# Kernel optimization log

Measured on AMD Instinct MI355X. Metric: run time of the kernel, lower is better.

Reference implementation:

```python
import jax, jax.numpy as jnp
import numpy as np

D_FEAT = 6
T = 64
HID = 128
N = 8192
EPS = 1e-5


def setup_inputs() -> dict:
    key = jax.random.key(0)
    ks = jax.random.split(key, 16)
    s = 0.08
    rn = lambda k, shape: jax.random.normal(k, shape, dtype=jnp.float32) * s
    return {
        "x": jax.random.normal(ks[0], (N, D_FEAT * T), dtype=jnp.float32),
        "w_ih0": rn(ks[1], (3 * HID, D_FEAT)),
        "w_hh0": rn(ks[2], (3 * HID, HID)),
        "b_ih0": rn(ks[3], (3 * HID,)),
        "b_hh0": rn(ks[4], (3 * HID,)),
        "w_ih1": rn(ks[5], (3 * HID, HID)),
        "w_hh1": rn(ks[6], (3 * HID, HID)),
        "b_ih1": rn(ks[7], (3 * HID,)),
        "b_hh1": rn(ks[8], (3 * HID,)),
        "bn1_g": jnp.ones((HID,), jnp.float32),
        "bn1_b": jnp.zeros((HID,), jnp.float32),
        "fc_w": rn(ks[9], (HID, HID)),
        "fc_b": rn(ks[10], (HID,)),
        "bn2_g": jnp.ones((HID,), jnp.float32),
        "bn2_b": jnp.zeros((HID,), jnp.float32),
        "fco_w": rn(ks[11], (1, HID)),
        "fco_b": rn(ks[12], (1,)),
    }


def _gru_layer(xs, w_ih, w_hh, b_ih, b_hh):
    # xs: [T, N, in] -> per-step hidden states [T, N, H] (torch nn.GRU math)
    H = w_hh.shape[1]
    gi_all = jnp.einsum('tni,gi->tng', xs, w_ih) + b_ih  # precompute input gates [T,N,3H]

    def step(h, gi):
        gh = h @ w_hh.T + b_hh
        i_r, i_z, i_n = jnp.split(gi, 3, axis=1)
        h_r, h_z, h_n = jnp.split(gh, 3, axis=1)
        r = jax.nn.sigmoid(i_r + h_r)
        z = jax.nn.sigmoid(i_z + h_z)
        n = jnp.tanh(i_n + r * h_n)
        h_new = (1.0 - z) * n + z * h
        return h_new, h_new

    h0 = jnp.zeros((xs.shape[1], H), dtype=xs.dtype)
    _, hs = jax.lax.scan(step, h0, gi_all)
    return hs


def _bn(x, g, b):
    # BatchNorm1d with track_running_stats=False: always uses batch stats
    mu = jnp.mean(x, axis=0)
    var = jnp.mean((x - mu) ** 2, axis=0)
    return (x - mu) * jax.lax.rsqrt(var + EPS) * g + b


def reference(x, w_ih0, w_hh0, b_ih0, b_hh0, w_ih1, w_hh1, b_ih1, b_hh1,
              bn1_g, bn1_b, fc_w, fc_b, bn2_g, bn2_b, fco_w, fco_b):
    n = x.shape[0]
    # reshape(N, d_feat, T).permute(0,2,1) -> time-major [T, N, d_feat] for scan
    xs = x.reshape(n, D_FEAT, T).transpose(2, 0, 1)
    h1 = _gru_layer(xs, w_ih0, w_hh0, b_ih0, b_hh0)
    h2 = _gru_layer(h1, w_ih1, w_hh1, b_ih1, b_hh1)
    hidden = _bn(h2[-1], bn1_g, bn1_b)  # [N, H]
    # cal_attention: mean_d(h_i * h_j) - mean(h_i)*mean(h_j)
    #   == (hidden @ hidden.T)/H - outer(row_means, row_means)  (exact identity)
    m = jnp.mean(hidden, axis=1)
    att = hidden @ hidden.T / jnp.float32(hidden.shape[1]) - jnp.outer(m, m)  # [N, N]
    out = att @ hidden              # [N, H]
    out = out @ fc_w.T + fc_b
    out = _bn(out, bn2_g, bn2_b)
    out = jax.nn.leaky_relu(out, 0.01)
    return (out @ fco_w.T + fco_b).squeeze(-1)  # [N]
```

## Files before the change

kernel.cpp:

```cpp
#include <hip/hip_runtime.h>

typedef unsigned short u16;
typedef short bf16x8 __attribute__((ext_vector_type(8)));
typedef float f32x4 __attribute__((ext_vector_type(4)));

#define NBATCH 8192

__device__ __forceinline__ f32x4 mfma16(bf16x8 a, bf16x8 b, f32x4 c) {
  return __builtin_amdgcn_mfma_f32_16x16x32_bf16(a, b, c, 0, 0, 0);
}
__device__ __forceinline__ u16 f2bf(float f) {
  unsigned int u = __float_as_uint(f);
  return (u16)((u + 0x7FFFu + ((u >> 16) & 1u)) >> 16);
}
__device__ __forceinline__ float bf2f(u16 h) {
  return __uint_as_float(((unsigned int)h) << 16);
}
__device__ __forceinline__ float sigm(float x) {
  return __builtin_amdgcn_rcpf(1.f + __builtin_amdgcn_exp2f(-1.44269504f * x));
}
__device__ __forceinline__ float tanh_(float x) {
  float t = __builtin_amdgcn_exp2f(2.88539008f * x);
  return 1.f - 2.f * __builtin_amdgcn_rcpf(t + 1.f);
}
__device__ __forceinline__ bf16x8 pack8(const float* p) {
  float4 a = *(const float4*)p, b = *(const float4*)(p + 4);
  bf16x8 r;
  r[0] = (short)f2bf(a.x); r[1] = (short)f2bf(a.y);
  r[2] = (short)f2bf(a.z); r[3] = (short)f2bf(a.w);
  r[4] = (short)f2bf(b.x); r[5] = (short)f2bf(b.y);
  r[6] = (short)f2bf(b.z); r[7] = (short)f2bf(b.w);
  return r;
}


#define A_WHH0 0
#define A_H0B  98304
#define A_XB   114688
#define A_LDS  118784

#define GRU0_STEP(RD, WR, T)                                                    \
  {                                                                             \
    if (xact && (T) < 63) {                                                     \
      u16 xh = f2bf(xv);                                                        \
      u16 xl = f2bf(xv - bf2f(xh));                                             \
      char* xw = sm + A_XB + (WR)*2048 + xm*64 + xd*2;                          \
      *(u16*)xw = xh; *(u16*)(xw + 16) = xl; *(u16*)(xw + 32) = xh;             \
      if ((T) < 62) xv = gx[(T) + 2];                                           \
    }                                                                           \
    f32x4 rz0[2][2], hn0[2], in0[2];                                            \
    _Pragma("unroll") for (int mt = 0; mt < 2; ++mt) {                          \
      rz0[mt][0] = (f32x4){brz0r, brz0r, brz0r, brz0r};                         \
      rz0[mt][1] = (f32x4){brz0z, brz0z, brz0z, brz0z};                         \
      hn0[mt] = (f32x4){bhn0, bhn0, bhn0, bhn0};                                \
      in0[mt] = (f32x4){bin0, bin0, bin0, bin0};                                \
    }                                                                           \
    _Pragma("unroll") for (int ki = 0; ki < 4; ++ki) {                          \
      bf16x8 a0 = *(bf16x8*)(sm + A_H0B + (RD)*8192 + arow0 + ad[ki]);          \
      bf16x8 a1 = *(bf16x8*)(sm + A_H0B + (RD)*8192 + arow1 + ad[ki]);          \
      bf16x8 b0 = *(bf16x8*)(sm + brow0 + ad[ki]);                              \
      bf16x8 b1 = *(bf16x8*)(sm + brow1 + ad[ki]);                              \
      bf16x8 b2 = *(bf16x8*)(sm + brow2 + ad[ki]);                              \
      rz0[0][0] = mfma16(a0, b0, rz0[0][0]);                                    \
      rz0[0][1] = mfma16(a0, b1, rz0[0][1]);                                    \
      hn0[0]    = mfma16(a0, b2, hn0[0]);                                       \
      rz0[1][0] = mfma16(a1, b0, rz0[1][0]);                                    \
      rz0[1][1] = mfma16(a1, b1, rz0[1][1]);                                    \
      hn0[1]    = mfma16(a1, b2, hn0[1]);                                       \
    }                                                                           \
    {                                                                           \
      bf16x8 ax0 = *(bf16x8*)(sm + A_XB + (RD)*2048 + xr0);                     \
      bf16x8 ax1 = *(bf16x8*)(sm + A_XB + (RD)*2048 + xr1);                     \
      rz0[0][0] = mfma16(ax0, wf0a, rz0[0][0]);                                 \
      rz0[0][1] = mfma16(ax0, wf0b, rz0[0][1]);                                 \
      in0[0]    = mfma16(ax0, wf0c, in0[0]);                                    \
      rz0[1][0] = mfma16(ax1, wf0a, rz0[1][0]);                                 \
      rz0[1][1] = mfma16(ax1, wf0b, rz0[1][1]);                                 \
      in0[1]    = mfma16(ax1, wf0c, in0[1]);                                    \
    }                                                                           \
    if ((T) >= 1) {       \
      uint4 gv = *(const uint4*)(sm + A_H0B + (RD)*8192 + tid*16);              \
      *(uint4*)(h0seq + (size_t)((T)-1)*2097152 + gofs) = gv;                   \
    }                                                                           \
    _Pragma("unroll") for (int mt = 0; mt < 2; ++mt)                            \
    _Pragma("unroll") for (int r = 0; r < 4; ++r) {                             \
      int s = mt*4 + r;                                                         \
      float rr = sigm(rz0[mt][0][r]);                                           \
      float zz = sigm(rz0[mt][1][r]);                                           \
      float nn = tanh_(__builtin_fmaf(rr, hn0[mt][r], in0[mt][r]));             \
      float h = h0s[s]; h = __builtin_fmaf(zz, h - nn, nn); h0s[s] = h;         \
      *(u16*)(sm + A_H0B + (WR)*8192 + st[s]) = f2bf(h);                        \
    }                                                                           \
    __syncthreads();                                                            \
  }

__global__ __attribute__((amdgpu_flat_work_group_size(512, 512)))
void k_gru0(const float* __restrict__ x,
            const float* __restrict__ wih0, const float* __restrict__ whh0,
            const float* __restrict__ bih0, const float* __restrict__ bhh0,
            char* __restrict__ h0seq) {
  extern __shared__ char sm[];
  const int tid = threadIdx.x;
  const int wid = tid >> 6;
  const int lane = tid & 63;
  const int lq = lane >> 4;
  const int ul = lane & 15;
  const int u  = wid * 16 + ul;
  const int n0 = blockIdx.x * 32;
  const int sx = (ul & 7) << 4;
  const int gofs = blockIdx.x * 8192 + tid * 16;

  for (int idx = tid; idx < 5120; idx += 512)
    *(float*)(sm + A_H0B + idx * 4) = 0.f;
  for (int idx = tid; idx < 12288; idx += 512) {
    int g = idx >> 5, c4 = (idx & 31) * 4;
    float4 v = *(const float4*)(whh0 + g * 128 + c4);
    unsigned int p0 = (unsigned int)f2bf(v.x) | ((unsigned int)f2bf(v.y) << 16);
    unsigned int p1 = (unsigned int)f2bf(v.z) | ((unsigned int)f2bf(v.w) << 16);
    unsigned int* dst = (unsigned int*)(sm + A_WHH0 + g * 256 + ((c4 * 2) ^ ((g & 7) << 4)));
    dst[0] = p0; dst[1] = p1;
  }

  bf16x8 wf0a, wf0b, wf0c;
  {
    u16 t0[8] = {0,0,0,0,0,0,0,0}, t1[8] = {0,0,0,0,0,0,0,0}, t2[8] = {0,0,0,0,0,0,0,0};
    u16* ts[3] = {t0, t1, t2};
#pragma unroll
    for (int i = 0; i < 3; ++i) {
      int g = u + 128 * i;
      if (lq < 2) {
        for (int d = 0; d < 6; ++d) ts[i][d] = f2bf(wih0[g * 6 + d]);
      } else if (lq == 2) {
        for (int d = 0; d < 6; ++d) {
          float w = wih0[g * 6 + d];
          u16 h = f2bf(w);
          ts[i][d] = f2bf(w - bf2f(h));
        }
      }
    }
    wf0a = *(bf16x8*)t0; wf0b = *(bf16x8*)t1; wf0c = *(bf16x8*)t2;
  }
  const float brz0r = bih0[u] + bhh0[u];
  const float brz0z = bih0[u + 128] + bhh0[u + 128];
  const float bin0 = bih0[u + 256], bhn0 = bhh0[u + 256];

  int ad[4];
#pragma unroll
  for (int ki = 0; ki < 4; ++ki) ad[ki] = (ki * 64 + lq * 16) ^ sx;
  const int arow0 = ul * 256, arow1 = arow0 + 4096;
  const int xr0 = ul * 64 + lq * 16, xr1 = xr0 + 1024;
  const int brow0 = A_WHH0 + u * 256;
  const int brow1 = A_WHH0 + (u + 128) * 256;
  const int brow2 = A_WHH0 + (u + 256) * 256;
  int st[8];
#pragma unroll
  for (int mt = 0; mt < 2; ++mt)
#pragma unroll
    for (int r = 0; r < 4; ++r) {
      int m = mt * 16 + lq * 4 + r;
      st[mt * 4 + r] = m * 256 + ((u * 2) ^ ((m & 7) << 4));
    }

  float h0s[8];
#pragma unroll
  for (int s = 0; s < 8; ++s) h0s[s] = 0.f;

  const int xm = tid / 6, xd = tid - 6 * xm;
  const bool xact = tid < 192;
  const float* gx = x + (size_t)(n0 + xm) * 384 + xd * 64;

  __syncthreads();

  float xv = 0.f;
  if (xact) {
    float x0 = gx[0];
    u16 h = f2bf(x0);
    u16 l = f2bf(x0 - bf2f(h));
    char* p = sm + A_XB + xm * 64 + xd * 2;
    *(u16*)p = h; *(u16*)(p + 16) = l; *(u16*)(p + 32) = h;
    xv = gx[1];
  }
  __syncthreads();

  for (int t = 0; t < 64; t += 2) {
    GRU0_STEP(0, 1, t)
    GRU0_STEP(1, 0, t + 1)
  }
  {
    uint4 gv = *(const uint4*)(sm + A_H0B + 0 * 8192 + tid * 16);
    *(uint4*)(h0seq + (size_t)63 * 2097152 + gofs) = gv;
  }
}

#define B_WHH1 0
#define B_H0IN 98304
#define B_H1B  114688
#define B_LDS  131072

#define GRU1_STEP(RD, WR, T)                                                    \
  {                                                                             \
    uint4 hv = {0u, 0u, 0u, 0u};                                                \
    if ((T) < 63) hv = *(const uint4*)(gsrc + (size_t)((T)+1)*2097152);         \
    f32x4 rz1[2][2], hn1[2], in1[2];                                            \
    _Pragma("unroll") for (int mt = 0; mt < 2; ++mt) {                          \
      rz1[mt][0] = (f32x4){brz1r, brz1r, brz1r, brz1r};                         \
      rz1[mt][1] = (f32x4){brz1z, brz1z, brz1z, brz1z};                         \
      hn1[mt] = (f32x4){bhn1, bhn1, bhn1, bhn1};                                \
      in1[mt] = (f32x4){bin1, bin1, bin1, bin1};                                \
    }                                                                           \
    _Pragma("unroll") for (int ki = 0; ki < 4; ++ki) {                          \
      bf16x8 p0 = *(bf16x8*)(sm + B_H0IN + (RD)*8192 + arow0 + ad[ki]);         \
      bf16x8 p1 = *(bf16x8*)(sm + B_H0IN + (RD)*8192 + arow1 + ad[ki]);         \
      bf16x8 q0 = *(bf16x8*)(sm + B_H1B + (RD)*8192 + arow0 + ad[ki]);          \
      bf16x8 q1 = *(bf16x8*)(sm + B_H1B + (RD)*8192 + arow1 + ad[ki]);          \
      bf16x8 w0 = *(bf16x8*)(sm + brow0 + ad[ki]);                              \
      bf16x8 w1 = *(bf16x8*)(sm + brow1 + ad[ki]);                              \
      bf16x8 w2 = *(bf16x8*)(sm + brow2 + ad[ki]);                              \
      rz1[0][0] = mfma16(p0, wih1f[0][ki], rz1[0][0]);                          \
      rz1[0][0] = mfma16(q0, w0, rz1[0][0]);                                    \
      rz1[0][1] = mfma16(p0, wih1f[1][ki], rz1[0][1]);                          \
      rz1[0][1] = mfma16(q0, w1, rz1[0][1]);                                    \
      in1[0]    = mfma16(p0, wih1f[2][ki], in1[0]);                             \
      hn1[0]    = mfma16(q0, w2, hn1[0]);                                       \
      rz1[1][0] = mfma16(p1, wih1f[0][ki], rz1[1][0]);                          \
      rz1[1][0] = mfma16(q1, w0, rz1[1][0]);                                    \
      rz1[1][1] = mfma16(p1, wih1f[1][ki], rz1[1][1]);                          \
      rz1[1][1] = mfma16(q1, w1, rz1[1][1]);                                    \
      in1[1]    = mfma16(p1, wih1f[2][ki], in1[1]);                             \
      hn1[1]    = mfma16(q1, w2, hn1[1]);                                       \
    }                                                                           \
    if ((T) < 63) *(uint4*)(sm + B_H0IN + (WR)*8192 + tid*16) = hv;             \
    _Pragma("unroll") for (int mt = 0; mt < 2; ++mt)                            \
    _Pragma("unroll") for (int r = 0; r < 4; ++r) {                             \
      int s = mt*4 + r;                                                         \
      float rr = sigm(rz1[mt][0][r]);                                           \
      float zz = sigm(rz1[mt][1][r]);                                           \
      float nn = tanh_(__builtin_fmaf(rr, hn1[mt][r], in1[mt][r]));             \
      float h = h1s[s]; h = __builtin_fmaf(zz, h - nn, nn); h1s[s] = h;         \
      *(u16*)(sm + B_H1B + (WR)*8192 + st[s]) = f2bf(h);                        \
    }                                                                           \
    __syncthreads();                                                            \
  }

__global__ __attribute__((amdgpu_flat_work_group_size(512, 512)))
void k_gru1(const float* __restrict__ wih1, const float* __restrict__ whh1,
            const float* __restrict__ bih1, const float* __restrict__ bhh1,
            const char* __restrict__ h0seq, float* __restrict__ hraw) {
  extern __shared__ char sm[];
  const int tid = threadIdx.x;
  const int wid = tid >> 6;
  const int lane = tid & 63;
  const int lq = lane >> 4;
  const int ul = lane & 15;
  const int u  = wid * 16 + ul;
  const int n0 = blockIdx.x * 32;
  const int sx = (ul & 7) << 4;
  const char* gsrc = h0seq + blockIdx.x * 8192 + tid * 16;

  for (int idx = tid; idx < 2048; idx += 512)
    *(float*)(sm + B_H1B + idx * 4) = 0.f;
  for (int idx = tid; idx < 12288; idx += 512) {
    int g = idx >> 5, c4 = (idx & 31) * 4;
    float4 v = *(const float4*)(whh1 + g * 128 + c4);
    unsigned int p0 = (unsigned int)f2bf(v.x) | ((unsigned int)f2bf(v.y) << 16);
    unsigned int p1 = (unsigned int)f2bf(v.z) | ((unsigned int)f2bf(v.w) << 16);
    unsigned int* dst = (unsigned int*)(sm + B_WHH1 + g * 256 + ((c4 * 2) ^ ((g & 7) << 4)));
    dst[0] = p0; dst[1] = p1;
  }
  {
    uint4 h0v = *(const uint4*)(gsrc);
    *(uint4*)(sm + B_H0IN + tid * 16) = h0v;
  }
  bf16x8 wih1f[3][4];
#pragma unroll
  for (int i = 0; i < 3; ++i) {
    int g = u + 128 * i;
#pragma unroll
    for (int ki = 0; ki < 4; ++ki)
      wih1f[i][ki] = pack8(wih1 + g * 128 + ki * 32 + lq * 8);
  }
  const float brz1r = bih1[u] + bhh1[u];
  const float brz1z = bih1[u + 128] + bhh1[u + 128];
  const float bin1 = bih1[u + 256], bhn1 = bhh1[u + 256];

  int ad[4];
#pragma unroll
  for (int ki = 0; ki < 4; ++ki) ad[ki] = (ki * 64 + lq * 16) ^ sx;
  const int arow0 = ul * 256, arow1 = arow0 + 4096;
  const int brow0 = B_WHH1 + u * 256;
  const int brow1 = B_WHH1 + (u + 128) * 256;
  const int brow2 = B_WHH1 + (u + 256) * 256;
  int st[8];
#pragma unroll
  for (int mt = 0; mt < 2; ++mt)
#pragma unroll
    for (int r = 0; r < 4; ++r) {
      int m = mt * 16 + lq * 4 + r;
      st[mt * 4 + r] = m * 256 + ((u * 2) ^ ((m & 7) << 4));
    }

  float h1s[8];
#pragma unroll
  for (int s = 0; s < 8; ++s) h1s[s] = 0.f;

  __syncthreads();

  for (int t = 0; t < 64; t += 2) {
    GRU1_STEP(0, 1, t)
    GRU1_STEP(1, 0, t + 1)
  }

#pragma unroll
  for (int mt = 0; mt < 2; ++mt)
#pragma unroll
    for (int r = 0; r < 4; ++r) {
      int m = mt * 16 + lq * 4 + r;
      hraw[(size_t)(n0 + m) * 128 + u] = h1s[mt * 4 + r];
    }
}

__global__ void k_bn1p(const float* __restrict__ hraw, float* __restrict__ p) {
  __shared__ float s0[256], s1[256];
  int tid = threadIdx.x, b = blockIdx.x;
  int f = tid & 127, r = tid >> 7;
  float s = 0.f, q = 0.f;
  for (int n = b * 64 + r; n < b * 64 + 64; n += 2) {
    float v = hraw[(size_t)n * 128 + f];
    s += v; q += v * v;
  }
  s0[tid] = s; s1[tid] = q;
  __syncthreads();
  if (tid < 128) {
    p[b * 256 + tid] = s0[tid] + s0[tid + 128];
    p[b * 256 + 128 + tid] = s1[tid] + s1[tid + 128];
  }
}

__global__ void k_bn1r(const float* __restrict__ p, float* __restrict__ mu1,
                       float* __restrict__ rs1) {
  int f = threadIdx.x;
  float s = 0.f, q = 0.f;
  for (int b = 0; b < 128; ++b) { s += p[b * 256 + f]; q += p[b * 256 + 128 + f]; }
  float mu = s / 8192.f, var = q / 8192.f - mu * mu;
  mu1[f] = mu; rs1[f] = rsqrtf(var + 1e-5f);
}

__global__ void k_attp(const float* __restrict__ hraw, const float* __restrict__ mu1,
                       const float* __restrict__ rs1, const float* __restrict__ g1,
                       const float* __restrict__ b1, float* __restrict__ hidden,
                       float* __restrict__ mvec, float* __restrict__ gpart,
                       float* __restrict__ mhpart) {
  __shared__ float hid[64][128];
  __shared__ float mld[64];
  int tid = threadIdx.x, blk = blockIdx.x, n0 = blk * 64;
  for (int idx = tid; idx < 64 * 128; idx += 256) {
    int n = idx >> 7, f = idx & 127;
    float v = (hraw[(size_t)(n0 + n) * 128 + f] - mu1[f]) * rs1[f] * g1[f] + b1[f];
    hid[n][f] = v;
    hidden[(size_t)(n0 + n) * 128 + f] = v;
  }
  __syncthreads();
  if (tid < 64) {
    float s = 0.f;
    for (int f = 0; f < 128; ++f) s += hid[tid][f];
    s *= (1.f / 128.f);
    mld[tid] = s; mvec[n0 + tid] = s;
  }
  __syncthreads();
  int i = tid >> 1, j0 = (tid & 1) * 64;
  float acc[64];
#pragma unroll
  for (int j = 0; j < 64; ++j) acc[j] = 0.f;
  for (int n = 0; n < 64; ++n) {
    float a = hid[n][i];
#pragma unroll
    for (int j = 0; j < 64; ++j) acc[j] += a * hid[n][j0 + j];
  }
#pragma unroll
  for (int j = 0; j < 64; ++j) gpart[(size_t)blk * 16384 + i * 128 + j0 + j] = acc[j];
  if (tid < 128) {
    float s = 0.f;
    for (int n = 0; n < 64; ++n) s += mld[n] * hid[n][tid];
    mhpart[blk * 128 + tid] = s;
  }
}

__global__ void k_attfa(const float* __restrict__ gpart, const float* __restrict__ mhpart,
                        float* __restrict__ gfull, float* __restrict__ mhfull) {
  int idx = blockIdx.x * 256 + threadIdx.x;
  float s = 0.f;
  for (int b = 0; b < 128; ++b) s += gpart[(size_t)b * 16384 + idx];
  gfull[idx] = s;
  if (blockIdx.x == 0 && threadIdx.x < 128) {
    float t = 0.f;
    for (int b = 0; b < 128; ++b) t += mhpart[b * 128 + threadIdx.x];
    mhfull[threadIdx.x] = t;
  }
}

__global__ void k_attfb(const float* __restrict__ gfull, const float* __restrict__ mhfull,
                        const float* __restrict__ fcw, float* __restrict__ m2,
                        float* __restrict__ uvec) {
  int idx = blockIdx.x * 128 + threadIdx.x;
  int k = idx >> 7, j = idx & 127;
  const float4* ga = (const float4*)(gfull + k * 128);
  const float4* fb = (const float4*)(fcw + j * 128);
  float a0 = 0.f, a1 = 0.f, a2 = 0.f, a3 = 0.f;
#pragma unroll 8
  for (int f = 0; f < 32; ++f) {
    float4 a = ga[f], b = fb[f];
    a0 += a.x * b.x; a1 += a.y * b.y; a2 += a.z * b.z; a3 += a.w * b.w;
  }
  m2[idx] = (a0 + a1 + a2 + a3) * (1.f / 128.f);
  if (idx < 128) {
    float s = 0.f;
    const float* fr = fcw + idx * 128;
#pragma unroll 8
    for (int f = 0; f < 128; ++f) s += mhfull[f] * fr[f];
    uvec[idx] = s;
  }
}

__global__ void k_out2(const float* __restrict__ hidden, const float* __restrict__ mvec,
                       const float* __restrict__ m2g, const float* __restrict__ uvec,
                       const float* __restrict__ fcb, float* __restrict__ out2,
                       float* __restrict__ bn2p) {
  extern __shared__ char smo[];
  float* m2l = (float*)smo;
  float* hl = m2l + 16384;
  float* ml = hl + 4096;
  float* red = ml + 32;
  int tid = threadIdx.x, blk = blockIdx.x, n0 = blk * 32;
  for (int idx = tid; idx < 16384; idx += 256) m2l[idx] = m2g[idx];
  for (int idx = tid; idx < 4096; idx += 256) hl[idx] = hidden[(size_t)n0 * 128 + idx];
  if (tid < 32) ml[tid] = mvec[n0 + tid];
  __syncthreads();
  int j = tid & 127, rg = tid >> 7;
  float uj = uvec[j], bj = fcb[j];
  float s1 = 0.f, s2 = 0.f;
  for (int q = 0; q < 16; ++q) {
    int nl = rg * 16 + q;
    float s = bj - ml[nl] * uj;
    const float* hr = hl + nl * 128;
#pragma unroll 8
    for (int k = 0; k < 128; ++k) s += hr[k] * m2l[k * 128 + j];
    out2[(size_t)(n0 + nl) * 128 + j] = s;
    s1 += s; s2 += s * s;
  }
  red[tid] = s1; red[256 + tid] = s2;
  __syncthreads();
  if (tid < 128) {
    bn2p[blk * 256 + tid] = red[tid] + red[128 + tid];
    bn2p[blk * 256 + 128 + tid] = red[256 + tid] + red[384 + tid];
  }
}

__global__ void k_bn2(const float* __restrict__ bn2p, float* __restrict__ mu2,
                      float* __restrict__ rs2) {
  int j = threadIdx.x;
  float s = 0.f, q = 0.f;
  for (int b = 0; b < 256; ++b) {
    s += bn2p[b * 256 + j];
    q += bn2p[b * 256 + 128 + j];
  }
  float mu = s / 8192.f, var = q / 8192.f - mu * mu;
  mu2[j] = mu; rs2[j] = rsqrtf(var + 1e-5f);
}

__global__ void k_fin(const float* __restrict__ out2, const float* __restrict__ mu2,
                      const float* __restrict__ rs2, const float* __restrict__ g2,
                      const float* __restrict__ b2, const float* __restrict__ fcow,
                      const float* __restrict__ fcob, float* __restrict__ y) {
  int tid = threadIdx.x, lane = tid & 63, w = tid >> 6;
  int n = blockIdx.x * 4 + w;
  float s = 0.f;
#pragma unroll
  for (int h = 0; h < 2; ++h) {
    int j = lane + h * 64;
    float v = (out2[(size_t)n * 128 + j] - mu2[j]) * rs2[j] * g2[j] + b2[j];
    v = fmaxf(v, 0.01f * v);
    s += v * fcow[j];
  }
  for (int off = 32; off; off >>= 1) s += __shfl_down(s, off);
  if (!lane) y[n] = s + fcob[0];
}

extern "C" void kernel_launch(void* const* d_in, const int* in_sizes, int n_in,
                              void* d_out, int out_size, void* d_ws, size_t ws_size,
                              hipStream_t stream) {
  const float* x    = (const float*)d_in[0];
  const float* wih0 = (const float*)d_in[1];
  const float* whh0 = (const float*)d_in[2];
  const float* bih0 = (const float*)d_in[3];
  const float* bhh0 = (const float*)d_in[4];
  const float* wih1 = (const float*)d_in[5];
  const float* whh1 = (const float*)d_in[6];
  const float* bih1 = (const float*)d_in[7];
  const float* bhh1 = (const float*)d_in[8];
  const float* g1   = (const float*)d_in[9];
  const float* b1   = (const float*)d_in[10];
  const float* fcw  = (const float*)d_in[11];
  const float* fcb  = (const float*)d_in[12];
  const float* g2   = (const float*)d_in[13];
  const float* b2   = (const float*)d_in[14];
  const float* fcow = (const float*)d_in[15];
  const float* fcob = (const float*)d_in[16];

  char* ws = (char*)d_ws;
  float* hraw   = (float*)(ws + 0);
  float* hidden = (float*)(ws + 4194304);
  float* mvec   = (float*)(ws + 8388608);
  float* mu1    = (float*)(ws + 8421376);
  float* rs1    = (float*)(ws + 8421888);
  float* gpart  = (float*)(ws + 8422400);
  float* mhpart = (float*)(ws + 16811008);
  float* m2     = (float*)(ws + 16876544);
  float* uvec   = (float*)(ws + 16942080);
  float* out2   = (float*)(ws + 16942592);
  float* bn2p   = (float*)(ws + 21136896);
  float* mu2    = (float*)(ws + 21399040);
  float* rs2    = (float*)(ws + 21399552);
  float* gfull  = (float*)(ws + 21400064);
  float* mhfull = (float*)(ws + 21465600);
  char*  h0seq  = (char*)(ws + 21495808);

  (void)hipFuncSetAttribute((const void*)k_gru0,
                            hipFuncAttributeMaxDynamicSharedMemorySize, A_LDS);
  (void)hipFuncSetAttribute((const void*)k_gru1,
                            hipFuncAttributeMaxDynamicSharedMemorySize, B_LDS);
  (void)hipFuncSetAttribute((const void*)k_out2,
                            hipFuncAttributeMaxDynamicSharedMemorySize, 84096);

  k_gru0<<<256, 512, A_LDS, stream>>>(x, wih0, whh0, bih0, bhh0, h0seq);
  k_gru1<<<256, 512, B_LDS, stream>>>(wih1, whh1, bih1, bhh1, h0seq, hraw);
  k_bn1p<<<128, 256, 0, stream>>>(hraw, bn2p);
  k_bn1r<<<1, 128, 0, stream>>>(bn2p, mu1, rs1);
  k_attp<<<128, 256, 0, stream>>>(hraw, mu1, rs1, g1, b1, hidden, mvec, gpart, mhpart);
  k_attfa<<<64, 256, 0, stream>>>(gpart, mhpart, gfull, mhfull);
  k_attfb<<<128, 128, 0, stream>>>(gfull, mhfull, fcw, m2, uvec);
  k_out2<<<256, 256, 84096, stream>>>(hidden, mvec, m2, uvec, fcb, out2, bn2p);
  k_bn2<<<1, 128, 0, stream>>>(bn2p, mu2, rs2);
  k_fin<<<2048, 256, 0, stream>>>(out2, mu2, rs2, g2, b2, fcow, fcob, (float*)d_out);
}
```

Baseline: 335.0 us.

## Halve GRU batch tile per block, keep n-gate weights in registers, double grid

Each GRU block now handles 16 sequences instead of 32, and the grid grows from 256 to 512 blocks. With 256 blocks only part of the device's compute units are busy during the serial 64-step recurrence. The n-gate hidden weights move from LDS into registers, which shrinks LDS per block and should allow more blocks per CU. In the second layer the h1 state goes from a double buffer to a single buffer guarded by an extra barrier each step. The trade-off is half the MFMA work per weight fragment, an additional __syncthreads per step in layer 1, and more register pressure.

```diff
diff --git a/kernel.cpp b/kernel.cpp
--- a/kernel.cpp
+++ b/kernel.cpp
@@ -34,62 +34,48 @@
 }
 
 
-#define A_WHH0 0
-#define A_H0B  98304
-#define A_XB   114688
-#define A_LDS  118784
+#define A_WRZ  0
+#define A_H0B  65536
+#define A_XB   73728
+#define A_LDS  75776
 
 #define GRU0_STEP(RD, WR, T)                                                    \
   {                                                                             \
     if (xact && (T) < 63) {                                                     \
       u16 xh = f2bf(xv);                                                        \
       u16 xl = f2bf(xv - bf2f(xh));                                             \
-      char* xw = sm + A_XB + (WR)*2048 + xm*64 + xd*2;                          \
+      char* xw = sm + A_XB + (WR)*1024 + xm*64 + xd*2;                          \
       *(u16*)xw = xh; *(u16*)(xw + 16) = xl; *(u16*)(xw + 32) = xh;             \
       if ((T) < 62) xv = gx[(T) + 2];                                           \
     }                                                                           \
-    f32x4 rz0[2][2], hn0[2], in0[2];                                            \
-    _Pragma("unroll") for (int mt = 0; mt < 2; ++mt) {                          \
-      rz0[mt][0] = (f32x4){brz0r, brz0r, brz0r, brz0r};                         \
-      rz0[mt][1] = (f32x4){brz0z, brz0z, brz0z, brz0z};                         \
-      hn0[mt] = (f32x4){bhn0, bhn0, bhn0, bhn0};                                \
-      in0[mt] = (f32x4){bin0, bin0, bin0, bin0};                                \
-    }                                                                           \
+    f32x4 accr = {brzr, brzr, brzr, brzr};                                      \
+    f32x4 accz = {brzz, brzz, brzz, brzz};                                      \
+    f32x4 acch = {bhn0, bhn0, bhn0, bhn0};                                      \
+    f32x4 acci = {bin0, bin0, bin0, bin0};                                      \
     _Pragma("unroll") for (int ki = 0; ki < 4; ++ki) {                          \
-      bf16x8 a0 = *(bf16x8*)(sm + A_H0B + (RD)*8192 + arow0 + ad[ki]);          \
-      bf16x8 a1 = *(bf16x8*)(sm + A_H0B + (RD)*8192 + arow1 + ad[ki]);          \
-      bf16x8 b0 = *(bf16x8*)(sm + brow0 + ad[ki]);                              \
-      bf16x8 b1 = *(bf16x8*)(sm + brow1 + ad[ki]);                              \
-      bf16x8 b2 = *(bf16x8*)(sm + brow2 + ad[ki]);                              \
-      rz0[0][0] = mfma16(a0, b0, rz0[0][0]);                                    \
-      rz0[0][1] = mfma16(a0, b1, rz0[0][1]);                                    \
-      hn0[0]    = mfma16(a0, b2, hn0[0]);                                       \
-      rz0[1][0] = mfma16(a1, b0, rz0[1][0]);                                    \
-      rz0[1][1] = mfma16(a1, b1, rz0[1][1]);                                    \
-      hn0[1]    = mfma16(a1, b2, hn0[1]);                                       \
+      bf16x8 a0 = *(bf16x8*)(sm + A_H0B + (RD)*4096 + arow0 + ad[ki]);          \
+      bf16x8 br = *(bf16x8*)(sm + A_WRZ + browr + ad[ki]);                      \
+      bf16x8 bz = *(bf16x8*)(sm + A_WRZ + browz + ad[ki]);                      \
+      accr = mfma16(a0, br, accr);                                              \
+      accz = mfma16(a0, bz, accz);                                              \
+      acch = mfma16(a0, wn0[ki], acch);                                         \
     }                                                                           \
     {                                                                           \
-      bf16x8 ax0 = *(bf16x8*)(sm + A_XB + (RD)*2048 + xr0);                     \
-      bf16x8 ax1 = *(bf16x8*)(sm + A_XB + (RD)*2048 + xr1);                     \
-      rz0[0][0] = mfma16(ax0, wf0a, rz0[0][0]);                                 \
-      rz0[0][1] = mfma16(ax0, wf0b, rz0[0][1]);                                 \
-      in0[0]    = mfma16(ax0, wf0c, in0[0]);                                    \
-      rz0[1][0] = mfma16(ax1, wf0a, rz0[1][0]);                                 \
-      rz0[1][1] = mfma16(ax1, wf0b, rz0[1][1]);                                 \
-      in0[1]    = mfma16(ax1, wf0c, in0[1]);                                    \
+      bf16x8 ax0 = *(bf16x8*)(sm + A_XB + (RD)*1024 + xr0);                     \
+      accr = mfma16(ax0, wf0a, accr);                                           \
+      accz = mfma16(ax0, wf0b, accz);                                           \
+      acci = mfma16(ax0, wf0c, acci);                                           \
     }                                                                           \
     if ((T) >= 1) {       \
-      uint4 gv = *(const uint4*)(sm + A_H0B + (RD)*8192 + tid*16);              \
-      *(uint4*)(h0seq + (size_t)((T)-1)*2097152 + gofs) = gv;                   \
-    }                                                                           \
-    _Pragma("unroll") for (int mt = 0; mt < 2; ++mt)                            \
+      uint2 gv = *(const uint2*)(sm + A_H0B + (RD)*4096 + tid*8);               \
+      *(uint2*)(h0seq + (size_t)((T)-1)*2097152 + gofs) = gv;                   \
+    }                                                                           \
     _Pragma("unroll") for (int r = 0; r < 4; ++r) {                             \
-      int s = mt*4 + r;                                                         \
-      float rr = sigm(rz0[mt][0][r]);                                           \
-      float zz = sigm(rz0[mt][1][r]);                                           \
-      float nn = tanh_(__builtin_fmaf(rr, hn0[mt][r], in0[mt][r]));             \
-      float h = h0s[s]; h = __builtin_fmaf(zz, h - nn, nn); h0s[s] = h;         \
-      *(u16*)(sm + A_H0B + (WR)*8192 + st[s]) = f2bf(h);                        \
+      float rr = sigm(accr[r]);                                                 \
+      float zz = sigm(accz[r]);                                                 \
+      float nn = tanh_(__builtin_fmaf(rr, acch[r], acci[r]));                   \
+      float h = h0s[r]; h = __builtin_fmaf(zz, h - nn, nn); h0s[r] = h;         \
+      *(u16*)(sm + A_H0B + (WR)*4096 + st[r]) = f2bf(h);                        \
     }                                                                           \
     __syncthreads();                                                            \
   }
@@ -106,20 +92,24 @@
   const int lq = lane >> 4;
   const int ul = lane & 15;
   const int u  = wid * 16 + ul;
-  const int n0 = blockIdx.x * 32;
+  const int n0 = blockIdx.x * 16;
   const int sx = (ul & 7) << 4;
-  const int gofs = blockIdx.x * 8192 + tid * 16;
-
-  for (int idx = tid; idx < 5120; idx += 512)
+  const int gofs = blockIdx.x * 4096 + tid * 8;
+
+  for (int idx = tid; idx < 2560; idx += 512)
     *(float*)(sm + A_H0B + idx * 4) = 0.f;
-  for (int idx = tid; idx < 12288; idx += 512) {
+  for (int idx = tid; idx < 8192; idx += 512) {
     int g = idx >> 5, c4 = (idx & 31) * 4;
     float4 v = *(const float4*)(whh0 + g * 128 + c4);
     unsigned int p0 = (unsigned int)f2bf(v.x) | ((unsigned int)f2bf(v.y) << 16);
     unsigned int p1 = (unsigned int)f2bf(v.z) | ((unsigned int)f2bf(v.w) << 16);
-    unsigned int* dst = (unsigned int*)(sm + A_WHH0 + g * 256 + ((c4 * 2) ^ ((g & 7) << 4)));
+    unsigned int* dst = (unsigned int*)(sm + A_WRZ + g * 256 + ((c4 * 2) ^ ((g & 7) << 4)));
     dst[0] = p0; dst[1] = p1;
   }
+  bf16x8 wn0[4];
+#pragma unroll
+  for (int ki = 0; ki < 4; ++ki)
+    wn0[ki] = pack8(whh0 + (256 + u) * 128 + ki * 32 + lq * 8);
 
   bf16x8 wf0a, wf0b, wf0c;
   {
@@ -140,33 +130,30 @@
     }
     wf0a = *(bf16x8*)t0; wf0b = *(bf16x8*)t1; wf0c = *(bf16x8*)t2;
   }
-  const float brz0r = bih0[u] + bhh0[u];
-  const float brz0z = bih0[u + 128] + bhh0[u + 128];
+  const float brzr = bih0[u] + bhh0[u];
+  const float brzz = bih0[u + 128] + bhh0[u + 128];
   const float bin0 = bih0[u + 256], bhn0 = bhh0[u + 256];
 
   int ad[4];
 #pragma unroll
   for (int ki = 0; ki < 4; ++ki) ad[ki] = (ki * 64 + lq * 16) ^ sx;
-  const int arow0 = ul * 256, arow1 = arow0 + 4096;
-  const int xr0 = ul * 64 + lq * 16, xr1 = xr0 + 1024;
-  const int brow0 = A_WHH0 + u * 256;
-  const int brow1 = A_WHH0 + (u + 128) * 256;
-  const int brow2 = A_WHH0 + (u + 256) * 256;
-  int st[8];
-#pragma unroll
-  for (int mt = 0; mt < 2; ++mt)
-#pragma unroll
-    for (int r = 0; r < 4; ++r) {
-      int m = mt * 16 + lq * 4 + r;
-      st[mt * 4 + r] = m * 256 + ((u * 2) ^ ((m & 7) << 4));
-    }
-
-  float h0s[8];
-#pragma unroll
-  for (int s = 0; s < 8; ++s) h0s[s] = 0.f;
+  const int arow0 = ul * 256;
+  const int xr0 = ul * 64 + lq * 16;
+  const int browr = u * 256;
+  const int browz = (u + 128) * 256;
+  int st[4];
+#pragma unroll
+  for (int r = 0; r < 4; ++r) {
+    int m = lq * 4 + r;
+    st[r] = m * 256 + ((u * 2) ^ ((m & 7) << 4));
+  }
+
+  float h0s[4];
+#pragma unroll
+  for (int r = 0; r < 4; ++r) h0s[r] = 0.f;
 
   const int xm = tid / 6, xd = tid - 6 * xm;
-  const bool xact = tid < 192;
+  const bool xact = tid < 96;
   const float* gx = x + (size_t)(n0 + xm) * 384 + xd * 64;
 
   __syncthreads();
@@ -187,59 +174,49 @@
     GRU0_STEP(1, 0, t + 1)
   }
   {
-    uint4 gv = *(const uint4*)(sm + A_H0B + 0 * 8192 + tid * 16);
-    *(uint4*)(h0seq + (size_t)63 * 2097152 + gofs) = gv;
-  }
-}
-
-#define B_WHH1 0
-#define B_H0IN 98304
-#define B_H1B  114688
-#define B_LDS  131072
-
-#define GRU1_STEP(RD, WR, T)                                                    \
+    uint2 gv = *(const uint2*)(sm + A_H0B + tid * 8);
+    *(uint2*)(h0seq + (size_t)63 * 2097152 + gofs) = gv;
+  }
+}
+
+#define B_WRZ  0
+#define B_H0IN 65536
+#define B_H1B  73728
+#define B_LDS  77824
+
+#define GRU1_STEP(P, T)                                                         \
   {                                                                             \
-    uint4 hv = {0u, 0u, 0u, 0u};                                                \
-    if ((T) < 63) hv = *(const uint4*)(gsrc + (size_t)((T)+1)*2097152);         \
-    f32x4 rz1[2][2], hn1[2], in1[2];                                            \
-    _Pragma("unroll") for (int mt = 0; mt < 2; ++mt) {                          \
-      rz1[mt][0] = (f32x4){brz1r, brz1r, brz1r, brz1r};                         \
-      rz1[mt][1] = (f32x4){brz1z, brz1z, brz1z, brz1z};                         \
-      hn1[mt] = (f32x4){bhn1, bhn1, bhn1, bhn1};                                \
-      in1[mt] = (f32x4){bin1, bin1, bin1, bin1};                                \
-    }                                                                           \
+    uint2 hv = {0u, 0u};                                                        \
+    if ((T) < 63) hv = *(const uint2*)(gsrc + (size_t)((T)+1)*2097152);         \
+    f32x4 accr = {brzr, brzr, brzr, brzr};                                      \
+    f32x4 accz = {brzz, brzz, brzz, brzz};                                      \
+    f32x4 acci = {bin1, bin1, bin1, bin1};                                      \
+    f32x4 acch = {bhn1, bhn1, bhn1, bhn1};                                      \
     _Pragma("unroll") for (int ki = 0; ki < 4; ++ki) {                          \
-      bf16x8 p0 = *(bf16x8*)(sm + B_H0IN + (RD)*8192 + arow0 + ad[ki]);         \
-      bf16x8 p1 = *(bf16x8*)(sm + B_H0IN + (RD)*8192 + arow1 + ad[ki]);         \
-      bf16x8 q0 = *(bf16x8*)(sm + B_H1B + (RD)*8192 + arow0 + ad[ki]);          \
-      bf16x8 q1 = *(bf16x8*)(sm + B_H1B + (RD)*8192 + arow1 + ad[ki]);          \
-      bf16x8 w0 = *(bf16x8*)(sm + brow0 + ad[ki]);                              \
-      bf16x8 w1 = *(bf16x8*)(sm + brow1 + ad[ki]);                              \
-      bf16x8 w2 = *(bf16x8*)(sm + brow2 + ad[ki]);                              \
-      rz1[0][0] = mfma16(p0, wih1f[0][ki], rz1[0][0]);                          \
-      rz1[0][0] = mfma16(q0, w0, rz1[0][0]);                                    \
-      rz1[0][1] = mfma16(p0, wih1f[1][ki], rz1[0][1]);                          \
-      rz1[0][1] = mfma16(q0, w1, rz1[0][1]);                                    \
-      in1[0]    = mfma16(p0, wih1f[2][ki], in1[0]);                             \
-      hn1[0]    = mfma16(q0, w2, hn1[0]);                                       \
-      rz1[1][0] = mfma16(p1, wih1f[0][ki], rz1[1][0]);                          \
-      rz1[1][0] = mfma16(q1, w0, rz1[1][0]);                                    \
-      rz1[1][1] = mfma16(p1, wih1f[1][ki], rz1[1][1]);                          \
-      rz1[1][1] = mfma16(q1, w1, rz1[1][1]);                                    \
-      in1[1]    = mfma16(p1, wih1f[2][ki], in1[1]);                             \
-      hn1[1]    = mfma16(q1, w2, hn1[1]);                                       \
-    }                                                                           \
-    if ((T) < 63) *(uint4*)(sm + B_H0IN + (WR)*8192 + tid*16) = hv;             \
-    _Pragma("unroll") for (int mt = 0; mt < 2; ++mt)                            \
+      bf16x8 p0 = *(bf16x8*)(sm + B_H0IN + (P)*4096 + arow0 + ad[ki]);          \
+      bf16x8 q0 = *(bf16x8*)(sm + B_H1B + arow0 + ad[ki]);                      \
+      bf16x8 br = *(bf16x8*)(sm + B_WRZ + browr + ad[ki]);                      \
+      bf16x8 bz = *(bf16x8*)(sm + B_WRZ + browz + ad[ki]);                      \
+      accr = mfma16(p0, wih1f[0][ki], accr);                                    \
+      accr = mfma16(q0, br, accr);                                              \
+      accz = mfma16(p0, wih1f[1][ki], accz);                                    \
+      accz = mfma16(q0, bz, accz);                                              \
+      acci = mfma16(p0, wih1f[2][ki], acci);                                    \
+      acch = mfma16(q0, wn1[ki], acch);                                         \
+    }                                                                           \
+    u16 hw[4];                                                                  \
     _Pragma("unroll") for (int r = 0; r < 4; ++r) {                             \
-      int s = mt*4 + r;                                                         \
-      float rr = sigm(rz1[mt][0][r]);                                           \
-      float zz = sigm(rz1[mt][1][r]);                                           \
-      float nn = tanh_(__builtin_fmaf(rr, hn1[mt][r], in1[mt][r]));             \
-      float h = h1s[s]; h = __builtin_fmaf(zz, h - nn, nn); h1s[s] = h;         \
-      *(u16*)(sm + B_H1B + (WR)*8192 + st[s]) = f2bf(h);                        \
-    }                                                                           \
-    __syncthreads();                                                            \
+      float rr = sigm(accr[r]);                                                 \
+      float zz = sigm(accz[r]);                                                 \
+      float nn = tanh_(__builtin_fmaf(rr, acch[r], acci[r]));                   \
+      float h = h1s[r]; h = __builtin_fmaf(zz, h - nn, nn); h1s[r] = h;         \
+      hw[r] = f2bf(h);                                                          \
+    }                                                                           \
+    __syncthreads();                 \
+    if ((T) < 63) *(uint2*)(sm + B_H0IN + ((P)^1)*4096 + tid*8) = hv;           \
+    _Pragma("unroll") for (int r = 0; r < 4; ++r)                               \
+      *(u16*)(sm + B_H1B + st[r]) = hw[r];                                      \
+    __syncthreads();                            \
   }
 
 __global__ __attribute__((amdgpu_flat_work_group_size(512, 512)))
@@ -253,25 +230,25 @@
   const int lq = lane >> 4;
   const int ul = lane & 15;
   const int u  = wid * 16 + ul;
-  const int n0 = blockIdx.x * 32;
+  const int n0 = blockIdx.x * 16;
   const int sx = (ul & 7) << 4;
-  const char* gsrc = h0seq + blockIdx.x * 8192 + tid * 16;
-
-  for (int idx = tid; idx < 2048; idx += 512)
+  const char* gsrc = h0seq + blockIdx.x * 4096 + tid * 8;
+
+  for (int idx = tid; idx < 1024; idx += 512)
     *(float*)(sm + B_H1B + idx * 4) = 0.f;
-  for (int idx = tid; idx < 12288; idx += 512) {
+  for (int idx = tid; idx < 8192; idx += 512) {
     int g = idx >> 5, c4 = (idx & 31) * 4;
     float4 v = *(const float4*)(whh1 + g * 128 + c4);
     unsigned int p0 = (unsigned int)f2bf(v.x) | ((unsigned int)f2bf(v.y) << 16);
     unsigned int p1 = (unsigned int)f2bf(v.z) | ((unsigned int)f2bf(v.w) << 16);
-    unsigned int* dst = (unsigned int*)(sm + B_WHH1 + g * 256 + ((c4 * 2) ^ ((g & 7) << 4)));
+    unsigned int* dst = (unsigned int*)(sm + B_WRZ + g * 256 + ((c4 * 2) ^ ((g & 7) << 4)));
     dst[0] = p0; dst[1] = p1;
   }
   {
-    uint4 h0v = *(const uint4*)(gsrc);
-    *(uint4*)(sm + B_H0IN + tid * 16) = h0v;
-  }
-  bf16x8 wih1f[3][4];
+    uint2 h0v = *(const uint2*)(gsrc);
+    *(uint2*)(sm + B_H0IN + tid * 8) = h0v;
+  }
+  bf16x8 wih1f[3][4], wn1[4];
 #pragma unroll
   for (int i = 0; i < 3; ++i) {
     int g = u + 128 * i;
@@ -279,44 +256,43 @@
     for (int ki = 0; ki < 4; ++ki)
       wih1f[i][ki] = pack8(wih1 + g * 128 + ki * 32 + lq * 8);
   }
-  const float brz1r = bih1[u] + bhh1[u];
-  const float brz1z = bih1[u + 128] + bhh1[u + 128];
+#pragma unroll
+  for (int ki = 0; ki < 4; ++ki)
+    wn1[ki] = pack8(whh1 + (256 + u) * 128 + ki * 32 + lq * 8);
+
+  const float brzr = bih1[u] + bhh1[u];
+  const float brzz = bih1[u + 128] + bhh1[u + 128];
   const float bin1 = bih1[u + 256], bhn1 = bhh1[u + 256];
 
   int ad[4];
 #pragma unroll
   for (int ki = 0; ki < 4; ++ki) ad[ki] = (ki * 64 + lq * 16) ^ sx;
-  const int arow0 = ul * 256, arow1 = arow0 + 4096;
-  const int brow0 = B_WHH1 + u * 256;
-  const int brow1 = B_WHH1 + (u + 128) * 256;
-  const int brow2 = B_WHH1 + (u + 256) * 256;
-  int st[8];
-#pragma unroll
-  for (int mt = 0; mt < 2; ++mt)
-#pragma unroll
-    for (int r = 0; r < 4; ++r) {
-      int m = mt * 16 + lq * 4 + r;
-      st[mt * 4 + r] = m * 256 + ((u * 2) ^ ((m & 7) << 4));
-    }
-
-  float h1s[8];
-#pragma unroll
-  for (int s = 0; s < 8; ++s) h1s[s] = 0.f;
+  const int arow0 = ul * 256;
+  const int browr = u * 256;
+  const int browz = (u + 128) * 256;
+  int st[4];
+#pragma unroll
+  for (int r = 0; r < 4; ++r) {
+    int m = lq * 4 + r;
+    st[r] = m * 256 + ((u * 2) ^ ((m & 7) << 4));
+  }
+
+  float h1s[4];
+#pragma unroll
+  for (int r = 0; r < 4; ++r) h1s[r] = 0.f;
 
   __syncthreads();
 
   for (int t = 0; t < 64; t += 2) {
-    GRU1_STEP(0, 1, t)
-    GRU1_STEP(1, 0, t + 1)
-  }
-
-#pragma unroll
-  for (int mt = 0; mt < 2; ++mt)
-#pragma unroll
-    for (int r = 0; r < 4; ++r) {
-      int m = mt * 16 + lq * 4 + r;
-      hraw[(size_t)(n0 + m) * 128 + u] = h1s[mt * 4 + r];
-    }
+    GRU1_STEP(0, t)
+    GRU1_STEP(1, t + 1)
+  }
+
+#pragma unroll
+  for (int r = 0; r < 4; ++r) {
+    int m = lq * 4 + r;
+    hraw[(size_t)(n0 + m) * 128 + u] = h1s[r];
+  }
 }
 
 __global__ void k_bn1p(const float* __restrict__ hraw, float* __restrict__ p) {
@@ -531,8 +507,8 @@
   (void)hipFuncSetAttribute((const void*)k_out2,
                             hipFuncAttributeMaxDynamicSharedMemorySize, 84096);
 
-  k_gru0<<<256, 512, A_LDS, stream>>>(x, wih0, whh0, bih0, bhh0, h0seq);
-  k_gru1<<<256, 512, B_LDS, stream>>>(wih1, whh1, bih1, bhh1, h0seq, hraw);
+  k_gru0<<<512, 512, A_LDS, stream>>>(x, wih0, whh0, bih0, bhh0, h0seq);
+  k_gru1<<<512, 512, B_LDS, stream>>>(wih1, whh1, bih1, bhh1, h0seq, hraw);
   k_bn1p<<<128, 256, 0, stream>>>(hraw, bn2p);
   k_bn1r<<<1, 128, 0, stream>>>(bn2p, mu1, rs1);
   k_attp<<<128, 256, 0, stream>>>(hraw, mu1, rs1, g1, b1, hidden, mvec, gpart, mhpart);
```

Measured after the change: 342.5 us. +2.2%, slower.
